# Optimization experiments

Hardware: AMD Instinct MI355X
Metric: run time of the kernel (lower is better)

## Reference

```python
import jax, jax.numpy as jnp
import numpy as np

N_HEAD = 12
LN_EPS = 1e-5


def _layernorm(x, g, b):
    m = jnp.mean(x, axis=-1, keepdims=True)
    v = jnp.mean(jnp.square(x - m), axis=-1, keepdims=True)
    return (x - m) * jax.lax.rsqrt(v + LN_EPS) * g + b


def _block(x, p):
    # p holds single-layer params. x: [B, S, D]
    B, S, D = x.shape
    Dh = D // N_HEAD
    h = _layernorm(x, p['ln1_g'], p['ln1_b'])
    q = (h @ p['wq'] + p['bq']).reshape(B, S, N_HEAD, Dh)
    k = (h @ p['wk'] + p['bk']).reshape(B, S, N_HEAD, Dh)
    v = (h @ p['wv'] + p['bv']).reshape(B, S, N_HEAD, Dh)
    scores = jnp.einsum('bqhd,bkhd->bhqk', q, k) / np.sqrt(Dh).astype(x.dtype)
    causal = jnp.tril(jnp.ones((S, S), dtype=bool))  # valid_nums = arange(1..S)
    scores = jnp.where(causal, scores, -jnp.inf)
    attn = jax.nn.softmax(scores, axis=-1)  # dropout is identity in eval
    o = jnp.einsum('bhqk,bkhd->bqhd', attn, v).reshape(B, S, D)
    x = x + o @ p['wo'] + p['bo']
    h2 = _layernorm(x, p['ln2_g'], p['ln2_b'])
    ff = jax.nn.gelu(h2 @ p['w1'] + p['b1'], approximate=False) @ p['w2'] + p['b2']
    return x + ff


def _gpt_forward(idx, wte, wpe, layer_params, lnf_g, lnf_b, lm_w):
    S = idx.shape[1]
    x = wte[idx] + wpe[None, :S, :]  # embd dropout is identity in eval
    x = jax.lax.scan(lambda c, p: (_block(c, p), None), x, layer_params)[0]
    x = _layernorm(x, lnf_g, lnf_b)
    return x @ lm_w  # logits [B, S, V]


def setup_inputs() -> dict:
    B, S, D, V, L, F = 4, 1024, 768, 50257, 12, 3072
    key = jax.random.key(0)
    ks = iter(jax.random.split(key, 24))
    std = 0.02
    std_proj = 0.02 / np.sqrt(2 * L)  # special init for w_o / FFN.linear2

    def w(shape, s=std):
        return jax.random.normal(next(ks), shape, jnp.float32) * s

    return dict(
        idx=jax.random.randint(next(ks), (B, S), 0, V),
        wte=w((V, D)), wpe=w((S, D)),
        ln1_g=jnp.ones((L, D)), ln1_b=jnp.zeros((L, D)),
        wq=w((L, D, D)), bq=jnp.zeros((L, D)),
        wk=w((L, D, D)), bk=jnp.zeros((L, D)),
        wv=w((L, D, D)), bv=jnp.zeros((L, D)),
        wo=w((L, D, D), std_proj), bo=jnp.zeros((L, D)),
        ln2_g=jnp.ones((L, D)), ln2_b=jnp.zeros((L, D)),
        w1=w((L, D, F)), b1=jnp.zeros((L, F)),
        w2=w((L, F, D), std_proj), b2=jnp.zeros((L, D)),
        lnf_g=jnp.ones((D,)), lnf_b=jnp.zeros((D,)),
        lm_w=w((D, V)),
    )


def reference(idx, wte, wpe, ln1_g, ln1_b, wq, bq, wk, bk, wv, bv, wo, bo,
              ln2_g, ln2_b, w1, b1, w2, b2, lnf_g, lnf_b, lm_w):
    layer_params = dict(ln1_g=ln1_g, ln1_b=ln1_b, wq=wq, bq=bq, wk=wk, bk=bk,
                        wv=wv, bv=bv, wo=wo, bo=bo, ln2_g=ln2_g, ln2_b=ln2_b,
                        w1=w1, b1=b1, w2=w2, b2=b2)
    return _gpt_forward(idx, wte, wpe, layer_params, lnf_g, lnf_b, lm_w)
```

## Files before the change

### kernel.cpp

```cpp
#include <hip/hip_runtime.h>
#include <hip/hip_bf16.h>

typedef __attribute__((ext_vector_type(8))) short short8;
typedef __attribute__((ext_vector_type(4))) float floatx4;

#define GLD16(g, l) __builtin_amdgcn_global_load_lds( \
    (__attribute__((address_space(1))) void*)(g),      \
    (__attribute__((address_space(3))) void*)(l), 16, 0, 0)

#define MFMA_BF16(a, b, c) __builtin_amdgcn_mfma_f32_16x16x32_bf16((a), (b), (c), 0, 0, 0)

__device__ __forceinline__ short f2bf(float f) {
  union { __hip_bfloat16 h; short s; } u;
  u.h = __float2bfloat16(f);
  return u.s;
}

__global__ __launch_bounds__(256)
void transpose_convert(const float* __restrict__ in, short* __restrict__ out,
                       const int K, const int N, const size_t inStride,
                       const size_t outStride) {
  in += blockIdx.z * inStride;
  out += blockIdx.z * outStride;
  __shared__ float tile[32][33];
  const int n0 = blockIdx.x * 32;
  const int k0 = blockIdx.y * 32;
  const int tx = threadIdx.x;
  const int ty = threadIdx.y;
#pragma unroll
  for (int i = 0; i < 4; ++i) {
    const int kk = ty + i * 8;
    const int nn = n0 + tx;
    tile[kk][tx] = (nn < N) ? in[(size_t)(k0 + kk) * N + nn] : 0.f;
  }
  __syncthreads();
#pragma unroll
  for (int i = 0; i < 4; ++i) {
    const int nn = ty + i * 8;
    out[(size_t)(n0 + nn) * K + k0 + tx] = f2bf(tile[tx][nn]);
  }
}

__global__ __launch_bounds__(256)
void embed_kernel(const int* __restrict__ idx, const float* __restrict__ wte,
                  const float* __restrict__ wpe, float* __restrict__ x) {
  const int row = blockIdx.x;
  const int tok = idx[row];
  const int s = row & 1023;
  const float* wt = wte + (size_t)tok * 768;
  const float* wp = wpe + (size_t)s * 768;
  float* xr = x + (size_t)row * 768;
  for (int c = threadIdx.x; c < 768; c += 256) xr[c] = wt[c] + wp[c];
}

__global__ __launch_bounds__(256)
void ln_kernel(const float* __restrict__ x, const float* __restrict__ g,
               const float* __restrict__ b, short* __restrict__ out) {
  const int row = blockIdx.x;
  const int t = threadIdx.x;
  const int wv = t >> 6, lane = t & 63;
  const float* xr = x + (size_t)row * 768;
  const float v0 = xr[t], v1 = xr[t + 256], v2 = xr[t + 512];
  __shared__ float red[4];
  float s = v0 + v1 + v2;
#pragma unroll
  for (int m = 1; m < 64; m <<= 1) s += __shfl_xor(s, m);
  if (lane == 0) red[wv] = s;
  __syncthreads();
  const float mean = (red[0] + red[1] + red[2] + red[3]) * (1.0f / 768.0f);
  __syncthreads();
  const float d0 = v0 - mean, d1 = v1 - mean, d2 = v2 - mean;
  float q = d0 * d0 + d1 * d1 + d2 * d2;
#pragma unroll
  for (int m = 1; m < 64; m <<= 1) q += __shfl_xor(q, m);
  if (lane == 0) red[wv] = q;
  __syncthreads();
  const float var = (red[0] + red[1] + red[2] + red[3]) * (1.0f / 768.0f);
  const float inv = rsqrtf(var + 1e-5f);
  short* orow = out + (size_t)row * 768;
  orow[t] = f2bf(d0 * inv * g[t] + b[t]);
  orow[t + 256] = f2bf(d1 * inv * g[t + 256] + b[t + 256]);
  orow[t + 512] = f2bf(d2 * inv * g[t + 512] + b[t + 512]);
}

enum { EPI_QKV = 0, EPI_RESID = 1, EPI_GELU = 2 };

template <int BM, int BN>
__device__ __forceinline__ void stage_tiles(const short* __restrict__ Ab,
                                            const short* __restrict__ Bb,
                                            const int K, const int kb,
                                            short* pa, short* pb,
                                            const int tid, const int wv) {
#pragma unroll
  for (int i = 0; i < BM / 32; ++i) {
    const int p = i * 256 + tid;
    const int rr = p >> 3, up = p & 7;
    GLD16(Ab + (size_t)rr * K + kb + ((up ^ (rr & 7)) << 3),
          pa + (i * 256 + wv * 64) * 8);
  }
#pragma unroll
  for (int i = 0; i < BN / 32; ++i) {
    const int p = i * 256 + tid;
    const int rr = p >> 3, up = p & 7;
    GLD16(Bb + (size_t)rr * K + kb + ((up ^ (rr & 7)) << 3),
          pb + (i * 256 + wv * 64) * 8);
  }
}

template <int BM, int BN, int EPI>
__global__ __launch_bounds__(256)
void gemm_kernel(const short* __restrict__ A, const short* __restrict__ Bt,
                 const int K,
                 const float* __restrict__ bias0, const float* __restrict__ bias1,
                 const float* __restrict__ bias2, float* __restrict__ fout,
                 short* __restrict__ bout0, short* __restrict__ bout1,
                 short* __restrict__ bout2) {
  constexpr int MF = BM / 32;
  constexpr int NF = BN / 32;
  __shared__ short sA[2][BM * 64];
  __shared__ short sB[2][BN * 64];
  const int tid = threadIdx.x;
  const int wv = tid >> 6;
  const int lane = tid & 63;
  const int lrow = lane & 15;
  const int lk8 = lane >> 4;
  const int m0 = blockIdx.x * BM;
  const int n0 = blockIdx.y * BN;
  const int wm = (wv >> 1) * (BM / 2);
  const int wn = (wv & 1) * (BN / 2);

  floatx4 acc[MF][NF];
#pragma unroll
  for (int m = 0; m < MF; ++m)
#pragma unroll
    for (int n = 0; n < NF; ++n) acc[m][n] = {0.f, 0.f, 0.f, 0.f};

  const short* Ab = A + (size_t)m0 * K;
  const short* Bb = Bt + (size_t)n0 * K;

  const int nk = K >> 6;
  stage_tiles<BM, BN>(Ab, Bb, K, 0, sA[0], sB[0], tid, wv);
  __syncthreads();

  int cur = 0;
  for (int kt = 0; kt < nk; ++kt) {
    if (kt + 1 < nk)
      stage_tiles<BM, BN>(Ab, Bb, K, (kt + 1) << 6, sA[cur ^ 1], sB[cur ^ 1],
                          tid, wv);
    const short* pa = sA[cur];
    const short* pb = sB[cur];
    short8 af[MF][2], bv[NF][2];
#pragma unroll
    for (int m = 0; m < MF; ++m)
#pragma unroll
      for (int ks = 0; ks < 2; ++ks)
        af[m][ks] = *(const short8*)(pa + (wm + m * 16 + lrow) * 64 +
                                     (((ks * 4 + lk8) ^ (lrow & 7)) << 3));
#pragma unroll
    for (int n = 0; n < NF; ++n)
#pragma unroll
      for (int ks = 0; ks < 2; ++ks)
        bv[n][ks] = *(const short8*)(pb + (wn + n * 16 + lrow) * 64 +
                                     (((ks * 4 + lk8) ^ (lrow & 7)) << 3));
#pragma unroll
    for (int m = 0; m < MF; ++m)
#pragma unroll
      for (int n = 0; n < NF; ++n) {
        acc[m][n] = MFMA_BF16(af[m][0], bv[n][0], acc[m][n]);
        acc[m][n] = MFMA_BF16(af[m][1], bv[n][1], acc[m][n]);
      }
    __syncthreads();
    cur ^= 1;
  }

#pragma unroll
  for (int m = 0; m < MF; ++m) {
#pragma unroll
    for (int n = 0; n < NF; ++n) {
#pragma unroll
      for (int r = 0; r < 4; ++r) {
        const float v = acc[m][n][r];
        const int gm = m0 + wm + m * 16 + lk8 * 4 + r;
        const int gn = n0 + wn + n * 16 + lrow;
        if (EPI == EPI_QKV) {
          const int sec = (gn >= 1536) ? 2 : (gn >= 768 ? 1 : 0);
          const int nn = gn - sec * 768;
          const int hh = nn >> 6, dh = nn & 63;
          const int bb = gm >> 10, srow = gm & 1023;
          if (sec == 0) {
            bout0[(((size_t)(bb * 12 + hh) * 1024 + srow) << 6) + dh] =
                f2bf((v + bias0[nn]) * 0.18033688f);
          } else if (sec == 1) {
            bout1[(((size_t)(bb * 12 + hh) * 1024 + srow) << 6) + dh] =
                f2bf(v + bias1[nn]);
          } else {
            bout2[(((size_t)(bb * 12 + hh) * 64 + dh) << 10) + srow] =
                f2bf(v + bias2[nn]);
          }
        } else if (EPI == EPI_RESID) {
          float* xp = fout + (size_t)gm * 768 + gn;
          *xp = *xp + v + bias0[gn];
        } else {
          const float tt = v + bias0[gn];
          const float gl = 0.5f * tt * (1.f + erff(tt * 0.70710678118654752f));
          bout0[(size_t)gm * 3072 + gn] = f2bf(gl);
        }
      }
    }
  }
}

__global__ __launch_bounds__(512, 4)
void gemm_lm_kernel(const short* __restrict__ A, const short* __restrict__ Bt,
                    float* __restrict__ fout) {
  __shared__ short sA[256 * 64];
  __shared__ short sB[128 * 64];
  const int K = 768;
  const int tid = threadIdx.x;
  const int wv = tid >> 6;
  const int lane = tid & 63;
  const int lrow = lane & 15;
  const int lk8 = lane >> 4;
  const int m0 = blockIdx.x * 256;
  const int n0 = blockIdx.y * 128;
  const int wm = (wv >> 1) * 64;
  const int wn = (wv & 1) * 64;

  floatx4 acc[4][4];
#pragma unroll
  for (int m = 0; m < 4; ++m)
#pragma unroll
    for (int n = 0; n < 4; ++n) acc[m][n] = {0.f, 0.f, 0.f, 0.f};

  const short* Ab = A + (size_t)m0 * K;
  const short* Bb = Bt + (size_t)n0 * K;

  const short* pA[4];
  const short* pB[2];
#pragma unroll
  for (int i = 0; i < 4; ++i) {
    const int p = i * 512 + tid;
    const int rr = p >> 3, up = p & 7;
    pA[i] = Ab + (size_t)rr * K + ((up ^ (rr & 7)) << 3);
  }
#pragma unroll
  for (int i = 0; i < 2; ++i) {
    const int p = i * 512 + tid;
    const int rr = p >> 3, up = p & 7;
    pB[i] = Bb + (size_t)rr * K + ((up ^ (rr & 7)) << 3);
  }

  const int arow = (wm + lrow) * 64;
  const int xr = (lrow & 7);

  for (int kt = 0; kt < 12; ++kt) {
#pragma unroll
    for (int i = 0; i < 4; ++i) {
      GLD16(pA[i], sA + (i * 512 + wv * 64) * 8);
      pA[i] += 64;
    }
#pragma unroll
    for (int i = 0; i < 2; ++i) {
      GLD16(pB[i], sB + (i * 512 + wv * 64) * 8);
      pB[i] += 64;
    }
    __syncthreads();

    short8 bvv[4][2];
#pragma unroll
    for (int n = 0; n < 4; ++n) {
      const int brow = (wn + n * 16 + lrow) * 64;
      bvv[n][0] = *(const short8*)(sB + brow + ((lk8 ^ xr) << 3));
      bvv[n][1] = *(const short8*)(sB + brow + (((4 + lk8) ^ xr) << 3));
    }
#pragma unroll
    for (int m = 0; m < 4; ++m) {
      const short8 a0 = *(const short8*)(sA + arow + m * 1024 + ((lk8 ^ xr) << 3));
      const short8 a1 =
          *(const short8*)(sA + arow + m * 1024 + (((4 + lk8) ^ xr) << 3));
#pragma unroll
      for (int n = 0; n < 4; ++n) {
        acc[m][n] = MFMA_BF16(a0, bvv[n][0], acc[m][n]);
        acc[m][n] = MFMA_BF16(a1, bvv[n][1], acc[m][n]);
      }
    }
    __syncthreads();
  }

#pragma unroll
  for (int m = 0; m < 4; ++m)
#pragma unroll
    for (int n = 0; n < 4; ++n)
#pragma unroll
      for (int r = 0; r < 4; ++r) {
        const int gm = m0 + wm + m * 16 + lk8 * 4 + r;
        const int gn = n0 + wn + n * 16 + lrow;
        if (gn < 50257) fout[(size_t)gm * 50257 + gn] = acc[m][n][r];
      }
}

__global__ __launch_bounds__(256)
void attn_kernel(const short* __restrict__ q, const short* __restrict__ k,
                 const short* __restrict__ vt, short* __restrict__ o) {
  __shared__ short sK[64 * 64];
  __shared__ short sV[64 * 64];
  const int bh = blockIdx.x;
  const int qi = 15 - blockIdx.y;
  const int tid = threadIdx.x;
  const int wv = tid >> 6, lane = tid & 63;
  const int lrow = lane & 15, lk8 = lane >> 4;
  const int q0 = qi * 64;
  const int qrow = q0 + wv * 16 + lrow;

  const short* qg = q + ((size_t)(bh * 1024 + qrow)) * 64 + lk8 * 8;
  const short8 qf0 = *(const short8*)qg;
  const short8 qf1 = *(const short8*)(qg + 32);

  float m_run = -1e30f, lsum = 0.f;
  floatx4 accO[4];
#pragma unroll
  for (int n = 0; n < 4; ++n) accO[n] = {0.f, 0.f, 0.f, 0.f};

  for (int t = 0; t <= qi; ++t) {
    const int k0 = t * 64;
#pragma unroll
    for (int i = 0; i < 2; ++i) {
      const int e = (i * 256 + tid) * 8;
      const int r = e >> 6, cc = e & 63;
      const int su = ((cc >> 3) ^ (r & 7)) << 3;
      *(short8*)(sK + r * 64 + su) =
          *(const short8*)(k + ((size_t)(bh * 1024 + k0 + r)) * 64 + cc);
      *(short8*)(sV + r * 64 + su) =
          *(const short8*)(vt + ((size_t)(bh * 64 + r)) * 1024 + k0 + cc);
    }
    __syncthreads();

    floatx4 accS[4];
#pragma unroll
    for (int n = 0; n < 4; ++n) accS[n] = {0.f, 0.f, 0.f, 0.f};
    const int rKb = ((lrow >> 2) << 3) + (lrow & 3);
#pragma unroll
    for (int ks = 0; ks < 2; ++ks) {
      const short8 qf = ks ? qf1 : qf0;
#pragma unroll
      for (int n = 0; n < 4; ++n) {
        const int rK = ((n >> 1) << 5) + ((n & 1) << 2) + rKb;
        const short8 kf =
            *(const short8*)(sK + rK * 64 + (((ks * 4 + lk8) ^ (rK & 7)) << 3));
        accS[n] = MFMA_BF16(kf, qf, accS[n]);
      }
    }

    float sv[4][4];
    float mx = -1e30f;
#pragma unroll
    for (int n = 0; n < 4; ++n)
#pragma unroll
      for (int r = 0; r < 4; ++r) {
        const int key = k0 + ((n >> 1) << 5) + (lk8 << 3) + ((n & 1) << 2) + r;
        float s = accS[n][r];
        s = (key > qrow) ? -1e30f : s;
        sv[n][r] = s;
        mx = fmaxf(mx, s);
      }
    mx = fmaxf(mx, __shfl_xor(mx, 16));
    mx = fmaxf(mx, __shfl_xor(mx, 32));
    const float mnew = fmaxf(m_run, mx);
    const float sf = exp2f(m_run - mnew);
    m_run = mnew;

    float rs = 0.f;
    unsigned int w[4][2];
#pragma unroll
    for (int n = 0; n < 4; ++n)
#pragma unroll
      for (int rp = 0; rp < 2; ++rp) {
        const float ea = exp2f(sv[n][2 * rp] - mnew);
        const float eb = exp2f(sv[n][2 * rp + 1] - mnew);
        rs += ea + eb;
        w[n][rp] = (unsigned int)(unsigned short)f2bf(ea) |
                   ((unsigned int)(unsigned short)f2bf(eb) << 16);
      }
    lsum = lsum * sf + rs;

    float sfq[4];
#pragma unroll
    for (int r = 0; r < 4; ++r)
      sfq[r] = __shfl(sf, (lane & 48) | (lk8 * 4 + r));
#pragma unroll
    for (int n = 0; n < 4; ++n)
#pragma unroll
      for (int r = 0; r < 4; ++r) accO[n][r] *= sfq[r];

    union { short8 s; unsigned int u[4]; } paf0, paf1;
#pragma unroll
    for (int tt = 0; tt < 4; ++tt) {
      paf0.u[tt] = w[tt >> 1][tt & 1];
      paf1.u[tt] = w[2 + (tt >> 1)][tt & 1];
    }

#pragma unroll
    for (int n = 0; n < 4; ++n) {
      const int dh = n * 16 + lrow;
      const short8 vf0 = *(const short8*)(sV + dh * 64 + ((lk8 ^ (dh & 7)) << 3));
      const short8 vf1 =
          *(const short8*)(sV + dh * 64 + (((4 + lk8) ^ (dh & 7)) << 3));
      accO[n] = MFMA_BF16(paf0.s, vf0, accO[n]);
      accO[n] = MFMA_BF16(paf1.s, vf1, accO[n]);
    }
    __syncthreads();
  }

  float ls = lsum;
  ls += __shfl_xor(ls, 16);
  ls += __shfl_xor(ls, 32);
  const float invown = 1.f / ls;
  float invq[4];
#pragma unroll
  for (int r = 0; r < 4; ++r)
    invq[r] = __shfl(invown, (lane & 48) | (lk8 * 4 + r));

  const int bb = bh / 12, hh = bh % 12;
#pragma unroll
  for (int n = 0; n < 4; ++n)
#pragma unroll
    for (int r = 0; r < 4; ++r) {
      const int row = q0 + wv * 16 + lk8 * 4 + r;
      const float ov = accO[n][r] * invq[r];
      o[((size_t)(bb * 1024 + row)) * 768 + hh * 64 + n * 16 + lrow] = f2bf(ov);
    }
}

extern "C" void kernel_launch(void* const* d_in, const int* in_sizes, int n_in,
                              void* d_out, int out_size, void* d_ws, size_t ws_size,
                              hipStream_t stream) {
  const int* idx = (const int*)d_in[0];
  const float* wte = (const float*)d_in[1];
  const float* wpe = (const float*)d_in[2];
  const float* ln1_g = (const float*)d_in[3];
  const float* ln1_b = (const float*)d_in[4];
  const float* wq = (const float*)d_in[5];
  const float* bq = (const float*)d_in[6];
  const float* wk = (const float*)d_in[7];
  const float* bk = (const float*)d_in[8];
  const float* wv = (const float*)d_in[9];
  const float* bv = (const float*)d_in[10];
  const float* wo = (const float*)d_in[11];
  const float* bo = (const float*)d_in[12];
  const float* ln2_g = (const float*)d_in[13];
  const float* ln2_b = (const float*)d_in[14];
  const float* w1 = (const float*)d_in[15];
  const float* b1 = (const float*)d_in[16];
  const float* w2 = (const float*)d_in[17];
  const float* b2 = (const float*)d_in[18];
  const float* lnf_g = (const float*)d_in[19];
  const float* lnf_b = (const float*)d_in[20];
  const float* lm_w = (const float*)d_in[21];
  float* out = (float*)d_out;

  char* base = (char*)d_ws;
  size_t off = 0;
  auto alloc = [&](size_t bytes) {
    char* r = base + off;
    off = (off + bytes + 255) & ~(size_t)255;
    return r;
  };
  short* lmT = (short*)alloc((size_t)50304 * 768 * 2);
  float* x = (float*)alloc((size_t)4096 * 768 * 4);
  short* h = (short*)alloc((size_t)4096 * 768 * 2);
  short* qb = (short*)alloc((size_t)4096 * 768 * 2);
  short* kb = (short*)alloc((size_t)4096 * 768 * 2);
  short* vtb = (short*)alloc((size_t)4096 * 768 * 2);
  short* ob = (short*)alloc((size_t)4096 * 768 * 2);
  short* ff = (short*)alloc((size_t)4096 * 3072 * 2);

  const size_t LW = 7077888;
  const size_t dd = (size_t)768 * 768;
  const bool big = (off + (size_t)12 * LW * 2 + 256 <= ws_size);
  short* wAll = nullptr;
  short *wqkvT = nullptr, *woT = nullptr, *w1T = nullptr, *w2T = nullptr;
  if (big) {
    wAll = (short*)alloc((size_t)12 * LW * 2);
  } else {
    wqkvT = (short*)alloc((size_t)2304 * 768 * 2);
    woT = (short*)alloc((size_t)768 * 768 * 2);
    w1T = (short*)alloc((size_t)3072 * 768 * 2);
    w2T = (short*)alloc((size_t)768 * 3072 * 2);
    if (off > ws_size) return;
  }

  const dim3 tb(32, 8);
  transpose_convert<<<dim3(1572, 24, 1), tb, 0, stream>>>(lm_w, lmT, 768, 50257, 0, 0);
  if (big) {
    transpose_convert<<<dim3(24, 24, 12), tb, 0, stream>>>(wq, wAll + 0, 768, 768, dd, LW);
    transpose_convert<<<dim3(24, 24, 12), tb, 0, stream>>>(wk, wAll + 589824, 768, 768, dd, LW);
    transpose_convert<<<dim3(24, 24, 12), tb, 0, stream>>>(wv, wAll + 1179648, 768, 768, dd, LW);
    transpose_convert<<<dim3(24, 24, 12), tb, 0, stream>>>(wo, wAll + 1769472, 768, 768, dd, LW);
    transpose_convert<<<dim3(96, 24, 12), tb, 0, stream>>>(w1, wAll + 2359296, 768, 3072,
                                                           (size_t)768 * 3072, LW);
    transpose_convert<<<dim3(24, 96, 12), tb, 0, stream>>>(w2, wAll + 4718592, 3072, 768,
                                                           (size_t)3072 * 768, LW);
  }
  embed_kernel<<<4096, 256, 0, stream>>>(idx, wte, wpe, x);

  for (int l = 0; l < 12; ++l) {
    const short *pQKV, *pWO, *pW1, *pW2;
    if (big) {
      short* wl = wAll + (size_t)l * LW;
      pQKV = wl;
      pWO = wl + 1769472;
      pW1 = wl + 2359296;
      pW2 = wl + 4718592;
    } else {
      transpose_convert<<<dim3(24, 24, 1), tb, 0, stream>>>(wq + l * dd, wqkvT, 768, 768, 0, 0);
      transpose_convert<<<dim3(24, 24, 1), tb, 0, stream>>>(wk + l * dd, wqkvT + dd, 768, 768, 0, 0);
      transpose_convert<<<dim3(24, 24, 1), tb, 0, stream>>>(wv + l * dd, wqkvT + 2 * dd, 768, 768, 0, 0);
      transpose_convert<<<dim3(24, 24, 1), tb, 0, stream>>>(wo + l * dd, woT, 768, 768, 0, 0);
      transpose_convert<<<dim3(96, 24, 1), tb, 0, stream>>>(w1 + (size_t)l * 768 * 3072, w1T, 768, 3072, 0, 0);
      transpose_convert<<<dim3(24, 96, 1), tb, 0, stream>>>(w2 + (size_t)l * 3072 * 768, w2T, 3072, 768, 0, 0);
      pQKV = wqkvT; pWO = woT; pW1 = w1T; pW2 = w2T;
    }

    ln_kernel<<<4096, 256, 0, stream>>>(x, ln1_g + l * 768, ln1_b + l * 768, h);
    gemm_kernel<128, 64, EPI_QKV><<<dim3(32, 36), 256, 0, stream>>>(
        h, pQKV, 768, bq + l * 768, bk + l * 768, bv + l * 768, nullptr, qb, kb, vtb);
    attn_kernel<<<dim3(48, 16), 256, 0, stream>>>(qb, kb, vtb, ob);
    gemm_kernel<64, 64, EPI_RESID><<<dim3(64, 12), 256, 0, stream>>>(
        ob, pWO, 768, bo + l * 768, nullptr, nullptr, x, nullptr, nullptr, nullptr);
    ln_kernel<<<4096, 256, 0, stream>>>(x, ln2_g + l * 768, ln2_b + l * 768, h);
    gemm_kernel<128, 64, EPI_GELU><<<dim3(32, 48), 256, 0, stream>>>(
        h, pW1, 768, b1 + l * 3072, nullptr, nullptr, nullptr, ff, nullptr, nullptr);
    gemm_kernel<64, 64, EPI_RESID><<<dim3(64, 12), 256, 0, stream>>>(
        ff, pW2, 3072, b2 + l * 768, nullptr, nullptr, x, nullptr, nullptr, nullptr);
  }

  ln_kernel<<<4096, 256, 0, stream>>>(x, lnf_g, lnf_b, h);
  gemm_lm_kernel<<<dim3(16, 393), 512, 0, stream>>>(h, lmT, out);
}
```

Measured before the change: 2.886 ms.

## Use 128x128 single-buffered tiles for QKV/FFN1 GEMMs with precomputed load pointers

The GEMM kernel gains a DBUF template flag so the QKV and FFN1 projections can run with 128x128 tiles in one LDS buffer, with a barrier-separated stage/compute loop. The other GEMMs keep 64x64 tiles with double buffering. Global load addresses are now computed once and advanced by pointer increments instead of recomputing swizzled offsets every k-step. Larger tiles raise operand reuse and halve the block count, but dropping double buffering exposes load latency, and the bigger accumulator array may cut occupancy.

```diff
diff --git a/kernel.cpp b/kernel.cpp
--- a/kernel.cpp
+++ b/kernel.cpp
@@ -85,29 +85,7 @@
 
 enum { EPI_QKV = 0, EPI_RESID = 1, EPI_GELU = 2 };
 
-template <int BM, int BN>
-__device__ __forceinline__ void stage_tiles(const short* __restrict__ Ab,
-                                            const short* __restrict__ Bb,
-                                            const int K, const int kb,
-                                            short* pa, short* pb,
-                                            const int tid, const int wv) {
-#pragma unroll
-  for (int i = 0; i < BM / 32; ++i) {
-    const int p = i * 256 + tid;
-    const int rr = p >> 3, up = p & 7;
-    GLD16(Ab + (size_t)rr * K + kb + ((up ^ (rr & 7)) << 3),
-          pa + (i * 256 + wv * 64) * 8);
-  }
-#pragma unroll
-  for (int i = 0; i < BN / 32; ++i) {
-    const int p = i * 256 + tid;
-    const int rr = p >> 3, up = p & 7;
-    GLD16(Bb + (size_t)rr * K + kb + ((up ^ (rr & 7)) << 3),
-          pb + (i * 256 + wv * 64) * 8);
-  }
-}
-
-template <int BM, int BN, int EPI>
+template <int BM, int BN, int DBUF, int EPI>
 __global__ __launch_bounds__(256)
 void gemm_kernel(const short* __restrict__ A, const short* __restrict__ Bt,
                  const int K,
@@ -117,8 +95,9 @@
                  short* __restrict__ bout2) {
   constexpr int MF = BM / 32;
   constexpr int NF = BN / 32;
-  __shared__ short sA[2][BM * 64];
-  __shared__ short sB[2][BN * 64];
+  constexpr int WMF = BM / 32 / ((BM == 128 && BN == 128) ? 1 : 1);
+  __shared__ short sA[DBUF + 1][BM * 64];
+  __shared__ short sB[DBUF + 1][BN * 64];
   const int tid = threadIdx.x;
   const int wv = tid >> 6;
   const int lane = tid & 63;
@@ -128,55 +107,91 @@
   const int n0 = blockIdx.y * BN;
   const int wm = (wv >> 1) * (BM / 2);
   const int wn = (wv & 1) * (BN / 2);
-
-  floatx4 acc[MF][NF];
-#pragma unroll
-  for (int m = 0; m < MF; ++m)
-#pragma unroll
-    for (int n = 0; n < NF; ++n) acc[m][n] = {0.f, 0.f, 0.f, 0.f};
-
-  const short* Ab = A + (size_t)m0 * K;
-  const short* Bb = Bt + (size_t)n0 * K;
-
-  const int nk = K >> 6;
-  stage_tiles<BM, BN>(Ab, Bb, K, 0, sA[0], sB[0], tid, wv);
-  __syncthreads();
-
-  int cur = 0;
-  for (int kt = 0; kt < nk; ++kt) {
-    if (kt + 1 < nk)
-      stage_tiles<BM, BN>(Ab, Bb, K, (kt + 1) << 6, sA[cur ^ 1], sB[cur ^ 1],
-                          tid, wv);
-    const short* pa = sA[cur];
-    const short* pb = sB[cur];
-    short8 af[MF][2], bv[NF][2];
-#pragma unroll
-    for (int m = 0; m < MF; ++m)
-#pragma unroll
-      for (int ks = 0; ks < 2; ++ks)
-        af[m][ks] = *(const short8*)(pa + (wm + m * 16 + lrow) * 64 +
-                                     (((ks * 4 + lk8) ^ (lrow & 7)) << 3));
-#pragma unroll
-    for (int n = 0; n < NF; ++n)
-#pragma unroll
-      for (int ks = 0; ks < 2; ++ks)
-        bv[n][ks] = *(const short8*)(pb + (wn + n * 16 + lrow) * 64 +
-                                     (((ks * 4 + lk8) ^ (lrow & 7)) << 3));
-#pragma unroll
-    for (int m = 0; m < MF; ++m)
-#pragma unroll
-      for (int n = 0; n < NF; ++n) {
+  constexpr int MW = BM / 2 / 16;
+  constexpr int NW = BN / 2 / 16;
+
+  floatx4 acc[MW][NW];
+#pragma unroll
+  for (int m = 0; m < MW; ++m)
+#pragma unroll
+    for (int n = 0; n < NW; ++n) acc[m][n] = {0.f, 0.f, 0.f, 0.f};
+
+  const short* pA[MF];
+  const short* pB[NF];
+#pragma unroll
+  for (int i = 0; i < MF; ++i) {
+    const int p = i * 256 + tid;
+    const int rr = p >> 3, up = p & 7;
+    pA[i] = A + (size_t)(m0 + rr) * K + ((up ^ (rr & 7)) << 3);
+  }
+#pragma unroll
+  for (int i = 0; i < NF; ++i) {
+    const int p = i * 256 + tid;
+    const int rr = p >> 3, up = p & 7;
+    pB[i] = Bt + (size_t)(n0 + rr) * K + ((up ^ (rr & 7)) << 3);
+  }
+
+  auto stage = [&](int buf) {
+#pragma unroll
+    for (int i = 0; i < MF; ++i) {
+      GLD16(pA[i], sA[buf] + (i * 256 + wv * 64) * 8);
+      pA[i] += 64;
+    }
+#pragma unroll
+    for (int i = 0; i < NF; ++i) {
+      GLD16(pB[i], sB[buf] + (i * 256 + wv * 64) * 8);
+      pB[i] += 64;
+    }
+  };
+
+  auto compute = [&](const short* pa, const short* pb) {
+    const int xr = lrow & 7;
+    short8 af[MW][2], bv[NW][2];
+#pragma unroll
+    for (int m = 0; m < MW; ++m) {
+      const int row = (wm + m * 16 + lrow) * 64;
+      af[m][0] = *(const short8*)(pa + row + ((lk8 ^ xr) << 3));
+      af[m][1] = *(const short8*)(pa + row + (((4 + lk8) ^ xr) << 3));
+    }
+#pragma unroll
+    for (int n = 0; n < NW; ++n) {
+      const int row = (wn + n * 16 + lrow) * 64;
+      bv[n][0] = *(const short8*)(pb + row + ((lk8 ^ xr) << 3));
+      bv[n][1] = *(const short8*)(pb + row + (((4 + lk8) ^ xr) << 3));
+    }
+#pragma unroll
+    for (int m = 0; m < MW; ++m)
+#pragma unroll
+      for (int n = 0; n < NW; ++n) {
         acc[m][n] = MFMA_BF16(af[m][0], bv[n][0], acc[m][n]);
         acc[m][n] = MFMA_BF16(af[m][1], bv[n][1], acc[m][n]);
       }
+  };
+
+  const int nk = K >> 6;
+  if (DBUF) {
+    stage(0);
     __syncthreads();
-    cur ^= 1;
-  }
-
-#pragma unroll
-  for (int m = 0; m < MF; ++m) {
-#pragma unroll
-    for (int n = 0; n < NF; ++n) {
+    int cur = 0;
+    for (int kt = 0; kt < nk; ++kt) {
+      if (kt + 1 < nk) stage(cur ^ 1);
+      compute(sA[cur], sB[cur]);
+      __syncthreads();
+      cur ^= 1;
+    }
+  } else {
+    for (int kt = 0; kt < nk; ++kt) {
+      stage(0);
+      __syncthreads();
+      compute(sA[0], sB[0]);
+      __syncthreads();
+    }
+  }
+
+#pragma unroll
+  for (int m = 0; m < MW; ++m) {
+#pragma unroll
+    for (int n = 0; n < NW; ++n) {
 #pragma unroll
       for (int r = 0; r < 4; ++r) {
         const float v = acc[m][n][r];
@@ -522,15 +537,15 @@
     }
 
     ln_kernel<<<4096, 256, 0, stream>>>(x, ln1_g + l * 768, ln1_b + l * 768, h);
-    gemm_kernel<128, 64, EPI_QKV><<<dim3(32, 36), 256, 0, stream>>>(
+    gemm_kernel<128, 128, 0, EPI_QKV><<<dim3(32, 18), 256, 0, stream>>>(
         h, pQKV, 768, bq + l * 768, bk + l * 768, bv + l * 768, nullptr, qb, kb, vtb);
     attn_kernel<<<dim3(48, 16), 256, 0, stream>>>(qb, kb, vtb, ob);
-    gemm_kernel<64, 64, EPI_RESID><<<dim3(64, 12), 256, 0, stream>>>(
+    gemm_kernel<64, 64, 1, EPI_RESID><<<dim3(64, 12), 256, 0, stream>>>(
         ob, pWO, 768, bo + l * 768, nullptr, nullptr, x, nullptr, nullptr, nullptr);
     ln_kernel<<<4096, 256, 0, stream>>>(x, ln2_g + l * 768, ln2_b + l * 768, h);
-    gemm_kernel<128, 64, EPI_GELU><<<dim3(32, 48), 256, 0, stream>>>(
+    gemm_kernel<128, 128, 0, EPI_GELU><<<dim3(32, 24), 256, 0, stream>>>(
         h, pW1, 768, b1 + l * 3072, nullptr, nullptr, nullptr, ff, nullptr, nullptr);
-    gemm_kernel<64, 64, EPI_RESID><<<dim3(64, 12), 256, 0, stream>>>(
+    gemm_kernel<64, 64, 1, EPI_RESID><<<dim3(64, 12), 256, 0, stream>>>(
         ff, pW2, 3072, b2 + l * 768, nullptr, nullptr, x, nullptr, nullptr, nullptr);
   }
 
```

New measurement: 2.997 ms. 1.04x slower.
